# Kernel optimization log

Hardware: AMD Instinct MI355X
Metric: run time of the kernel (lower is better)

Reference implementation:

```python
import jax, jax.numpy as jnp
import numpy as np

DIM = 1024
HEADS = 16
HDIM = DIM // HEADS
HIDDEN = 4 * DIM
SCALE = HDIM ** -0.5


def layernorm(x, g, b, eps=1e-5):
    mu = jnp.mean(x, axis=-1, keepdims=True)
    var = jnp.var(x, axis=-1, keepdims=True)
    return (x - mu) * jax.lax.rsqrt(var + eps) * g + b


def setup_inputs() -> dict:
    key = jax.random.key(0)
    ks = jax.random.split(key, 8)
    s = 0.02
    return {
        "x": jax.random.normal(ks[0], (4, 1024, DIM), dtype=jnp.float32),
        "ln1_g": jnp.ones((DIM,), jnp.float32),
        "ln1_b": jnp.zeros((DIM,), jnp.float32),
        "ln2_g": jnp.ones((DIM,), jnp.float32),
        "ln2_b": jnp.zeros((DIM,), jnp.float32),
        "qkv_w": jax.random.normal(ks[1], (DIM, 3 * DIM), jnp.float32) * s,
        "qkv_b": jnp.zeros((3 * DIM,), jnp.float32),
        "proj_w": jax.random.normal(ks[2], (DIM, DIM), jnp.float32) * s,
        "proj_b": jnp.zeros((DIM,), jnp.float32),
        "fc1_w": jax.random.normal(ks[3], (DIM, HIDDEN), jnp.float32) * s,
        "fc1_b": jnp.zeros((HIDDEN,), jnp.float32),
        "fc2_w": jax.random.normal(ks[4], (HIDDEN, DIM), jnp.float32) * s,
        "fc2_b": jnp.zeros((DIM,), jnp.float32),
    }


def reference(x, ln1_g, ln1_b, ln2_g, ln2_b, qkv_w, qkv_b, proj_w, proj_b,
              fc1_w, fc1_b, fc2_w, fc2_b):
    B, N, C = x.shape
    # --- attention branch ---
    h = layernorm(x, ln1_g, ln1_b)
    qkv = h @ qkv_w + qkv_b                       # [B,N,3C]
    qkv = qkv.reshape(B, N, 3, HEADS, HDIM)
    q, k, v = jnp.moveaxis(qkv, 2, 0)             # each [B,N,H,Dh]
    q = jnp.swapaxes(q, 1, 2)                      # [B,H,N,Dh]
    k = jnp.swapaxes(k, 1, 2)
    v = jnp.swapaxes(v, 1, 2)
    attn = jnp.einsum('bhqd,bhkd->bhqk', q, k) * SCALE
    attn = jax.nn.softmax(attn, axis=-1)
    o = jnp.einsum('bhqk,bhkd->bhqd', attn, v)     # [B,H,N,Dh]
    o = jnp.swapaxes(o, 1, 2).reshape(B, N, C)
    x = x + (o @ proj_w + proj_b)
    # --- MLP branch ---
    h = layernorm(x, ln2_g, ln2_b)
    h = jax.nn.gelu(h @ fc1_w + fc1_b, approximate=False)
    x = x + (h @ fc2_w + fc2_b)
    return x
```

## Files before the change

kernel.cpp:

```cpp
#include <hip/hip_runtime.h>
#include <math.h>

#define DIM    1024
#define HEADS  16
#define HDIM   64
#define HIDDEN 4096
#define BATCH  4
#define SEQ    1024
#define ROWS   (BATCH * SEQ)

typedef short s16x8 __attribute__((ext_vector_type(8)));
typedef float f32x4 __attribute__((ext_vector_type(4)));

__device__ __forceinline__ float blo(unsigned int u) {
    union { unsigned int i; float f; } x; x.i = u << 16; return x.f;
}
__device__ __forceinline__ float bhi(unsigned int u) {
    union { unsigned int i; float f; } x; x.i = u & 0xffff0000u; return x.f;
}
__device__ __forceinline__ unsigned short f2b(float f) {
    union { float f; unsigned int i; } x; x.f = f;
    unsigned int r = x.i + 0x7fffu + ((x.i >> 16) & 1u);
    return (unsigned short)(r >> 16);
}

__device__ __forceinline__ float gelu_f(float x) {
    float z  = fabsf(x) * 0.70710678118f;
    float t  = __builtin_amdgcn_rcpf(__builtin_fmaf(0.3275911f, z, 1.0f));
    float p  = ((((1.061405429f * t - 1.453152027f) * t + 1.421413741f) * t
                 - 0.284496736f) * t + 0.254829592f) * t;
    float e  = exp2f(-0.72134752f * x * x);
    float w  = 0.5f * p * e;
    float phi = (x >= 0.0f) ? (1.0f - w) : w;
    return x * phi;
}

__device__ __forceinline__ size_t tidx(int row, int k, int Kdim) {
    return ((size_t)(row >> 4) * (Kdim >> 5) + (k >> 5)) * 512
         + (size_t)(((k & 31) >> 3) * 128 + (row & 15) * 8 + (k & 7));
}

__device__ __forceinline__ void gload_lds16(const void* g, void* l) {
    __builtin_amdgcn_global_load_lds(
        (const __attribute__((address_space(1))) unsigned int*)g,
        (__attribute__((address_space(3))) unsigned int*)l, 16, 0, 0);
}

__global__ __launch_bounds__(256) void prep_kernel(const float* __restrict__ x,
                                                   const float* __restrict__ g,
                                                   const float* __restrict__ b,
                                                   unsigned short* __restrict__ lnout,
                                                   const float* __restrict__ qkv_w,
                                                   unsigned short* __restrict__ wT_qkv,
                                                   const float* __restrict__ proj_w,
                                                   unsigned short* __restrict__ wT_proj,
                                                   const float* __restrict__ fc1_w,
                                                   unsigned short* __restrict__ wT_fc1,
                                                   const float* __restrict__ fc2_w,
                                                   unsigned short* __restrict__ wT_fc2) {
    __shared__ float red1[256], red2[256];
    __shared__ unsigned short T[64][68];
    const int bid = blockIdx.x;
    const int t = threadIdx.x;

    if (bid < ROWS) {
        int row = bid;
        const float* xr = x + (size_t)row * DIM;
        float4 v = *((const float4*)(xr + t * 4));
        float s  = v.x + v.y + v.z + v.w;
        float ss = v.x * v.x + v.y * v.y + v.z * v.z + v.w * v.w;
        red1[t] = s; red2[t] = ss;
        __syncthreads();
        for (int off = 128; off > 0; off >>= 1) {
            if (t < off) { red1[t] += red1[t + off]; red2[t] += red2[t + off]; }
            __syncthreads();
        }
        float mu   = red1[0] * (1.0f / DIM);
        float var  = red2[0] * (1.0f / DIM) - mu * mu;
        float rstd = rsqrtf(var + 1e-5f);
        float4 gv = *((const float4*)(g + t * 4));
        float4 bv = *((const float4*)(b + t * 4));
        ushort4 o;
        o.x = f2b((v.x - mu) * rstd * gv.x + bv.x);
        o.y = f2b((v.y - mu) * rstd * gv.y + bv.y);
        o.z = f2b((v.z - mu) * rstd * gv.z + bv.z);
        o.w = f2b((v.w - mu) * rstd * gv.w + bv.w);
        *((ushort4*)(lnout + tidx(row, t * 4, DIM))) = o;
    } else {
        int tt = bid - ROWS;
        const float* W; unsigned short* Wt; int K, N, bx, by;
        if (tt < 768) {
            W = qkv_w; Wt = wT_qkv; K = DIM; N = 3 * DIM; bx = tt % 48; by = tt / 48;
        } else if (tt < 768 + 256) {
            tt -= 768;
            W = proj_w; Wt = wT_proj; K = DIM; N = DIM; bx = tt % 16; by = tt / 16;
        } else if (tt < 768 + 256 + 1024) {
            tt -= 768 + 256;
            W = fc1_w; Wt = wT_fc1; K = DIM; N = HIDDEN; bx = tt % 64; by = tt / 64;
        } else {
            tt -= 768 + 256 + 1024;
            W = fc2_w; Wt = wT_fc2; K = HIDDEN; N = DIM; bx = tt % 16; by = tt / 16;
        }
        int n0 = bx * 64, k0 = by * 64;
        int cr = t >> 4;
        int cc = (t & 15) * 4;
        #pragma unroll
        for (int r = 0; r < 4; ++r) {
            int kk = cr + 16 * r;
            float4 v = *((const float4*)(W + (size_t)(k0 + kk) * N + n0 + cc));
            T[cc + 0][kk] = f2b(v.x);
            T[cc + 1][kk] = f2b(v.y);
            T[cc + 2][kk] = f2b(v.z);
            T[cc + 3][kk] = f2b(v.w);
        }
        __syncthreads();
        {
            int nn = t >> 2;
            int kg = (t & 3) * 16;
            #pragma unroll
            for (int p = 0; p < 2; ++p) {
                int k8 = kg + p * 8;
                ushort4 lo = *((ushort4*)&T[nn][k8]);
                ushort4 hi = *((ushort4*)&T[nn][k8 + 4]);
                unsigned short* dst = Wt + tidx(n0 + nn, k0 + k8, K);
                *((ushort4*)dst)       = lo;
                *((ushort4*)(dst + 4)) = hi;
            }
        }
    }
}

__global__ __launch_bounds__(256) void reduce_ln(const unsigned short* __restrict__ p0,
                                                 const unsigned short* __restrict__ p1,
                                                 const float* __restrict__ x,
                                                 const float* __restrict__ bias,
                                                 const float* __restrict__ g,
                                                 const float* __restrict__ b,
                                                 float* __restrict__ xout,
                                                 unsigned short* __restrict__ lnout) {
    int row = blockIdx.x;
    int t = threadIdx.x;
    size_t i = (size_t)row * DIM + t * 4;
    float4 xv = *((const float4*)(x + i));
    float4 bi = *((const float4*)(bias + t * 4));
    uint2 w0 = *((const uint2*)(p0 + i));
    uint2 w1 = *((const uint2*)(p1 + i));
    float4 v;
    v.x = xv.x + bi.x + blo(w0.x) + blo(w1.x);
    v.y = xv.y + bi.y + bhi(w0.x) + bhi(w1.x);
    v.z = xv.z + bi.z + blo(w0.y) + blo(w1.y);
    v.w = xv.w + bi.w + bhi(w0.y) + bhi(w1.y);
    *((float4*)(xout + i)) = v;

    float s  = v.x + v.y + v.z + v.w;
    float ss = v.x * v.x + v.y * v.y + v.z * v.z + v.w * v.w;
    __shared__ float red1[256], red2[256];
    red1[t] = s; red2[t] = ss;
    __syncthreads();
    for (int off = 128; off > 0; off >>= 1) {
        if (t < off) { red1[t] += red1[t + off]; red2[t] += red2[t + off]; }
        __syncthreads();
    }
    float mu   = red1[0] * (1.0f / DIM);
    float var  = red2[0] * (1.0f / DIM) - mu * mu;
    float rstd = rsqrtf(var + 1e-5f);
    float4 gv = *((const float4*)(g + t * 4));
    float4 bv = *((const float4*)(b + t * 4));
    ushort4 o;
    o.x = f2b((v.x - mu) * rstd * gv.x + bv.x);
    o.y = f2b((v.y - mu) * rstd * gv.y + bv.y);
    o.z = f2b((v.z - mu) * rstd * gv.z + bv.z);
    o.w = f2b((v.w - mu) * rstd * gv.w + bv.w);
    *((ushort4*)(lnout + tidx(row, t * 4, DIM))) = o;
}

__global__ __launch_bounds__(256, 4) void mfma_gemm(const unsigned short* __restrict__ A,
                                                 const unsigned short* __restrict__ Bt,
                                                 const float* __restrict__ bias,
                                                 void* __restrict__ Cout,
                                                 unsigned short* __restrict__ vt,
                                                 unsigned short* __restrict__ p0,
                                                 unsigned short* __restrict__ p1,
                                                 unsigned short* __restrict__ p2,
                                                 unsigned short* __restrict__ p3,
                                                 int M, int N, int K, int Ksplit, int fuse) {
    __shared__ __align__(16) short Asm[2][4096];
    __shared__ __align__(16) short Bsm[2][4096];

    const int tid  = threadIdx.x;
    const int lane = tid & 63;
    const int wave = tid >> 6;
    const int wy = wave >> 1, wx = wave & 1;
    const int lr = lane & 15;
    const int lq = lane >> 4;

    int m_t, n_t;
    {
        const int mt = gridDim.x, ntl = gridDim.y, G = 8;
        if (ntl > G) {
            int lin = blockIdx.y * mt + blockIdx.x;
            int gsz = mt * G;
            int grp = lin / gsz;
            int rem = lin - grp * gsz;
            m_t = rem % mt;
            n_t = grp * G + rem / mt;
        } else { m_t = blockIdx.x; n_t = blockIdx.y; }
    }
    const int m0 = m_t * 128, n0 = n_t * 128;
    const int kbase = blockIdx.z * Ksplit;
    const int kch = K >> 5;

    f32x4 acc[4][4];
    #pragma unroll
    for (int i = 0; i < 4; ++i)
        #pragma unroll
        for (int j = 0; j < 4; ++j)
            acc[i][j] = (f32x4){0.f, 0.f, 0.f, 0.f};

    const unsigned short* ag[2]; const unsigned short* bg[2];
    #pragma unroll
    for (int j = 0; j < 2; ++j) {
        int rc = wave * 2 + j;
        ag[j] = A  + ((size_t)((m0 >> 4) + rc) * kch + (kbase >> 5)) * 512 + lane * 8;
        bg[j] = Bt + ((size_t)((n0 >> 4) + rc) * kch + (kbase >> 5)) * 512 + lane * 8;
    }

#define STAGE(buf) { \
    _Pragma("unroll") for (int j_ = 0; j_ < 2; ++j_) { \
        gload_lds16(ag[j_], &Asm[buf][(wave * 2 + j_) * 512]); \
        gload_lds16(bg[j_], &Bsm[buf][(wave * 2 + j_) * 512]); \
        ag[j_] += 512; bg[j_] += 512; \
    } }
#define COMPUTE(buf) { \
    s16x8 af[4], bf[4]; \
    _Pragma("unroll") for (int i_ = 0; i_ < 4; ++i_) \
        af[i_] = *((const s16x8*)&Asm[buf][(wy * 4 + i_) * 512 + lane * 8]); \
    _Pragma("unroll") for (int j_ = 0; j_ < 4; ++j_) \
        bf[j_] = *((const s16x8*)&Bsm[buf][(wx * 4 + j_) * 512 + lane * 8]); \
    _Pragma("unroll") for (int i_ = 0; i_ < 4; ++i_) \
        _Pragma("unroll") for (int j_ = 0; j_ < 4; ++j_) \
            acc[i_][j_] = __builtin_amdgcn_mfma_f32_16x16x32_bf16(af[i_], bf[j_], acc[i_][j_], 0, 0, 0); \
    }

    STAGE(0);
    __syncthreads();
    for (int k0 = 0; k0 < Ksplit; k0 += 64) {
        STAGE(1);
        COMPUTE(0);
        __syncthreads();
        if (k0 + 64 < Ksplit) STAGE(0);
        COMPUTE(1);
        __syncthreads();
    }
#undef STAGE
#undef COMPUTE

    short* Wl = (wave < 2 ? (short*)Asm : (short*)Bsm) + (wave & 1) * 4096;

    if (fuse == 0 && vt && (n0 + wx * 64) >= 2 * DIM) {
        #pragma unroll
        for (int j = 0; j < 4; ++j) {
            int col = n0 + wx * 64 + j * 16 + lr;
            float bi = bias[col];
            #pragma unroll
            for (int i = 0; i < 4; ++i) {
                int row0 = m0 + wy * 64 + i * 16 + lq * 4;
                #pragma unroll
                for (int r = 0; r < 4; ++r) {
                    float val = acc[i][j][r] + bi;
                    int row = row0 + r;
                    int b_ = row >> 10, tok = row & 1023;
                    int hd = col - 2 * DIM, h_ = hd >> 6, d = hd & 63;
                    size_t o = (size_t)(b_ * 16 + h_) * 65536
                             + ((size_t)(d >> 4) * 32 + (tok >> 5)) * 512
                             + ((tok & 31) >> 3) * 128 + (d & 15) * 8 + (tok & 7);
                    vt[o] = f2b(val);
                }
            }
        }
    } else if (fuse == 3) {
        #pragma unroll
        for (int j = 0; j < 4; ++j) {
            #pragma unroll
            for (int i = 0; i < 4; ++i) {
                #pragma unroll
                for (int r = 0; r < 4; ++r) {
                    int rowL = i * 16 + lq * 4 + r;
                    int colL = (j * 16 + lr) ^ ((rowL & 7) << 3);
                    Wl[rowL * 64 + colL] = (short)f2b(acc[i][j][r]);
                }
            }
        }
        int z = blockIdx.z;
        unsigned short* P = (z == 0) ? p0 : (z == 1) ? p1 : (z == 2) ? p2 : p3;
        unsigned short* Prow = P + (size_t)(m0 + wy * 64 + lane) * N + n0 + wx * 64;
        #pragma unroll
        for (int c = 0; c < 8; ++c) {
            int colr = (c * 8) ^ ((lane & 7) << 3);
            s16x8 v = *((const s16x8*)&Wl[lane * 64 + colr]);
            *((s16x8*)&Prow[c * 8]) = v;
        }
    } else {
        #pragma unroll
        for (int j = 0; j < 4; ++j) {
            float bi = bias[n0 + wx * 64 + j * 16 + lr];
            #pragma unroll
            for (int i = 0; i < 4; ++i) {
                #pragma unroll
                for (int r = 0; r < 4; ++r) {
                    float val = acc[i][j][r] + bi;
                    if (fuse == 1) val = gelu_f(val);
                    int colL = (j & 1) * 16 + lr;
                    int hi = colL >> 3;
                    int pos = hi * 128 + (lq * 4 + r) * 8 + (lr & 7);
                    pos ^= ((pos >> 7) & 3) << 3;
                    Wl[(i * 2 + (j >> 1)) * 512 + pos] = (short)f2b(val);
                }
            }
        }
        const size_t rc0 = (size_t)((m0 + wy * 64) >> 4);
        const size_t cc0 = (size_t)((n0 + wx * 64) >> 5);
        const size_t nch = (size_t)(N >> 5);
        #pragma unroll
        for (int c = 0; c < 8; ++c) {
            int raddr = lane * 8;
            raddr ^= ((raddr >> 7) & 3) << 3;
            s16x8 v = *((const s16x8*)&Wl[c * 512 + raddr]);
            size_t chunk = (rc0 + (c >> 1)) * nch + cc0 + (c & 1);
            *((s16x8*)&((unsigned short*)Cout)[chunk * 512 + lane * 8]) = v;
        }
    }
}

__global__ __launch_bounds__(256) void reduce_kernel(const unsigned short* __restrict__ p0,
                                                     const unsigned short* __restrict__ p1,
                                                     const unsigned short* __restrict__ p2,
                                                     const unsigned short* __restrict__ p3,
                                                     int S,
                                                     const float* __restrict__ x,
                                                     const float* __restrict__ bias,
                                                     float* __restrict__ out) {
    int i = (blockIdx.x * 256 + threadIdx.x) * 8;
    int col = i & (DIM - 1);
    float4 b0 = *((const float4*)(bias + col));
    float4 b1 = *((const float4*)(bias + col + 4));
    float4 x0 = *((const float4*)(x + i));
    float4 x1 = *((const float4*)(x + i + 4));
    float a[8] = {x0.x + b0.x, x0.y + b0.y, x0.z + b0.z, x0.w + b0.w,
                  x1.x + b1.x, x1.y + b1.y, x1.z + b1.z, x1.w + b1.w};
    const unsigned short* ps[4] = {p0, p1, p2, p3};
    for (int s = 0; s < S; ++s) {
        uint4 w = *((const uint4*)(ps[s] + i));
        a[0] += blo(w.x); a[1] += bhi(w.x);
        a[2] += blo(w.y); a[3] += bhi(w.y);
        a[4] += blo(w.z); a[5] += bhi(w.z);
        a[6] += blo(w.w); a[7] += bhi(w.w);
    }
    *((float4*)(out + i))     = make_float4(a[0], a[1], a[2], a[3]);
    *((float4*)(out + i + 4)) = make_float4(a[4], a[5], a[6], a[7]);
}

__global__ __launch_bounds__(256, 6) void fattn_mfma(const unsigned short* __restrict__ qkv,
                                                  const unsigned short* __restrict__ Vt,
                                                  unsigned short* __restrict__ out) {
    __shared__ __align__(16) short Ks[4096];
    __shared__ __align__(16) short Vs[4096];
    __shared__ __align__(16) short Ps[64 * 72];
    __shared__ __align__(16) short OnesB[512];

    const int tid = threadIdx.x, lane = tid & 63, wave = tid >> 6;
    const int lr = lane & 15, lq = lane >> 4;
    const int L = blockIdx.x;
    const int idx = L >> 3;
    const int qt = idx & 15;
    const int bh = (L & 7) + 8 * (idx >> 4);
    const int b = bh >> 4, h = bh & 15;
    const int q0 = qt * 64;

    {
        s16x8 z = (s16x8){0,0,0,0,0,0,0,0};
        if (lr == 0) { z[0] = (short)0x3F80; z[1] = (short)0x3F80;
                       z[2] = (short)0x3F80; z[3] = (short)0x3F80;
                       z[4] = (short)0x3F80; z[5] = (short)0x3F80;
                       z[6] = (short)0x3F80; z[7] = (short)0x3F80; }
        if (wave == 0) *((s16x8*)&OnesB[lane * 8]) = z;
    }

    s16x8 aq[2];
    #pragma unroll
    for (int j = 0; j < 2; ++j) {
        const unsigned short* g = qkv + ((size_t)(((b * SEQ + q0) >> 4) + wave) * 96
                                         + 2 * h + j) * 512 + lane * 8;
        aq[j] = *((const s16x8*)g);
    }

    const unsigned short* kg_[2]; const unsigned short* vg_[2];
    short *kl_[2], *vl_[2];
    #pragma unroll
    for (int j = 0; j < 2; ++j) {
        int cid = wave * 2 + j;
        kg_[j] = qkv + ((size_t)(((b * SEQ) >> 4) + (cid >> 1)) * 96
                        + 32 + 2 * h + (cid & 1)) * 512 + lane * 8;
        vg_[j] = Vt + (size_t)bh * 65536
                 + ((size_t)(cid >> 1) * 32 + (cid & 1)) * 512 + lane * 8;
        kl_[j] = &Ks[cid * 512];
        vl_[j] = &Vs[cid * 512];
    }

    f32x4 osum[5];
    #pragma unroll
    for (int d = 0; d < 5; ++d)
        osum[d] = (f32x4){0.f, 0.f, 0.f, 0.f};

    const float c = 0.125f * 1.44269504f;

    for (int k0 = 0; k0 < SEQ; k0 += 64) {
        #pragma unroll
        for (int j = 0; j < 2; ++j) {
            gload_lds16(kg_[j], kl_[j]);
            gload_lds16(vg_[j], vl_[j]);
            kg_[j] += 4 * 96 * 512;
            vg_[j] += 1024;
        }
        __syncthreads();

        f32x4 s[4];
        #pragma unroll
        for (int jb = 0; jb < 4; ++jb)
            s[jb] = (f32x4){0.f, 0.f, 0.f, 0.f};
        __builtin_amdgcn_s_setprio(1);
        #pragma unroll
        for (int kc = 0; kc < 2; ++kc) {
            #pragma unroll
            for (int jb = 0; jb < 4; ++jb) {
                s16x8 bk = *((const s16x8*)&Ks[(jb * 2 + kc) * 512 + lane * 8]);
                s[jb] = __builtin_amdgcn_mfma_f32_16x16x32_bf16(aq[kc], bk, s[jb], 0, 0, 0);
            }
        }
        __builtin_amdgcn_s_setprio(0);

        #pragma unroll
        for (int r = 0; r < 4; ++r) {
            int prow = wave * 16 + lq * 4 + r;
            #pragma unroll
            for (int jb = 0; jb < 4; ++jb)
                Ps[prow * 72 + jb * 16 + lr] = (short)f2b(exp2f(s[jb][r] * c));
        }

        __builtin_amdgcn_s_setprio(1);
        #pragma unroll
        for (int kc = 0; kc < 2; ++kc) {
            s16x8 ap = *((const s16x8*)&Ps[(wave * 16 + lr) * 72 + kc * 32 + lq * 8]);
            #pragma unroll
            for (int db = 0; db < 4; ++db) {
                s16x8 bv = *((const s16x8*)&Vs[(db * 2 + kc) * 512 + lane * 8]);
                osum[db] = __builtin_amdgcn_mfma_f32_16x16x32_bf16(ap, bv, osum[db], 0, 0, 0);
            }
            s16x8 bo = *((const s16x8*)&OnesB[lane * 8]);
            osum[4] = __builtin_amdgcn_mfma_f32_16x16x32_bf16(ap, bo, osum[4], 0, 0, 0);
        }
        __builtin_amdgcn_s_setprio(0);
        __syncthreads();
    }

    {
        int qrow = q0 + wave * 16 + lq * 4;
        #pragma unroll
        for (int r = 0; r < 4; ++r) {
            float lsum = __shfl(osum[4][r], lane & 48, 64);
            float inv = 1.0f / lsum;
            int row = b * SEQ + qrow + r;
            #pragma unroll
            for (int db = 0; db < 4; ++db)
                out[tidx(row, h * 64 + db * 16 + lr, DIM)] = f2b(osum[db][r] * inv);
        }
    }
}

extern "C" void kernel_launch(void* const* d_in, const int* in_sizes, int n_in,
                              void* d_out, int out_size, void* d_ws, size_t ws_size,
                              hipStream_t stream) {
    const float* x      = (const float*)d_in[0];
    const float* ln1_g  = (const float*)d_in[1];
    const float* ln1_b  = (const float*)d_in[2];
    const float* ln2_g  = (const float*)d_in[3];
    const float* ln2_b  = (const float*)d_in[4];
    const float* qkv_w  = (const float*)d_in[5];
    const float* qkv_b  = (const float*)d_in[6];
    const float* proj_w = (const float*)d_in[7];
    const float* proj_b = (const float*)d_in[8];
    const float* fc1_w  = (const float*)d_in[9];
    const float* fc1_b  = (const float*)d_in[10];
    const float* fc2_w  = (const float*)d_in[11];
    const float* fc2_b  = (const float*)d_in[12];
    float* out = (float*)d_out;

    char* ws = (char*)d_ws;
    unsigned short* wT_fc2  = (unsigned short*)(ws);
    unsigned short* wT_qkv  = (unsigned short*)(ws + (8u  << 20));
    unsigned short* wT_proj = (unsigned short*)(ws + (14u << 20));
    unsigned short* qkvbuf  = (unsigned short*)(ws + (16u << 20));
    unsigned short* Vt      = (unsigned short*)(ws + (40u << 20));
    unsigned short* attnout = (unsigned short*)(ws + (48u << 20));
    unsigned short* lnout   = (unsigned short*)(ws + (56u << 20));
    unsigned short* wT_fc1  = (unsigned short*)(ws + (64u << 20));
    unsigned short* gelu    = (unsigned short*)(ws + (16u << 20));
    unsigned short* pp0 = (unsigned short*)(ws + (16u << 20));
    unsigned short* pp1 = (unsigned short*)(ws + (24u << 20));
    unsigned short* fp0 = (unsigned short*)(ws + (48u << 20));
    unsigned short* fp1 = (unsigned short*)(ws + (56u << 20));
    unsigned short* fp2 = (unsigned short*)(ws + (64u << 20));
    unsigned short* fp3 = (unsigned short*)(ws + (8u  << 20));

    prep_kernel<<<ROWS + 3072, 256, 0, stream>>>(
        x, ln1_g, ln1_b, lnout,
        qkv_w, wT_qkv, proj_w, wT_proj, fc1_w, wT_fc1, fc2_w, wT_fc2);
    mfma_gemm<<<dim3(ROWS / 128, 3 * DIM / 128, 1), 256, 0, stream>>>(
        lnout, wT_qkv, qkv_b, qkvbuf, Vt, nullptr, nullptr, nullptr, nullptr,
        ROWS, 3 * DIM, DIM, DIM, 0);
    fattn_mfma<<<(SEQ / 64) * BATCH * HEADS, 256, 0, stream>>>(qkvbuf, Vt, attnout);
    mfma_gemm<<<dim3(ROWS / 128, DIM / 128, 2), 256, 0, stream>>>(
        attnout, wT_proj, proj_b, nullptr, nullptr, pp0, pp1, nullptr, nullptr,
        ROWS, DIM, DIM, DIM / 2, 3);
    reduce_ln<<<ROWS, 256, 0, stream>>>(pp0, pp1, x, proj_b, ln2_g, ln2_b, out, lnout);
    mfma_gemm<<<dim3(ROWS / 128, HIDDEN / 128, 1), 256, 0, stream>>>(
        lnout, wT_fc1, fc1_b, gelu, nullptr, nullptr, nullptr, nullptr, nullptr,
        ROWS, HIDDEN, DIM, DIM, 1);
    mfma_gemm<<<dim3(ROWS / 128, DIM / 128, 4), 256, 0, stream>>>(
        gelu, wT_fc2, fc2_b, nullptr, nullptr, fp0, fp1, fp2, fp3,
        ROWS, DIM, HIDDEN, HIDDEN / 4, 3);
    reduce_kernel<<<ROWS * DIM / 2048, 256, 0, stream>>>(
        fp0, fp1, fp2, fp3, 4, out, fc2_b, out);
}
```

Measured before the change: 332.8 us.

## Atomic split-K fc2 epilogue, LDS-staged V store, double-buffered 32-key attention

```diff
diff --git a/kernel.cpp b/kernel.cpp
--- a/kernel.cpp
+++ b/kernel.cpp
@@ -181,8 +181,6 @@
                                                  unsigned short* __restrict__ vt,
                                                  unsigned short* __restrict__ p0,
                                                  unsigned short* __restrict__ p1,
-                                                 unsigned short* __restrict__ p2,
-                                                 unsigned short* __restrict__ p3,
                                                  int M, int N, int K, int Ksplit, int fuse) {
     __shared__ __align__(16) short Asm[2][4096];
     __shared__ __align__(16) short Bsm[2][4096];
@@ -258,24 +256,43 @@
     short* Wl = (wave < 2 ? (short*)Asm : (short*)Bsm) + (wave & 1) * 4096;
 
     if (fuse == 0 && vt && (n0 + wx * 64) >= 2 * DIM) {
+        int b_ = (m0 + wy * 64) >> 10;
+        int tok0 = (m0 + wy * 64) & 1023;
+        int h_ = (n0 + wx * 64 - 2 * DIM) >> 6;
+        #pragma unroll
+        for (int j = 0; j < 4; ++j) {
+            float bi = bias[n0 + wx * 64 + j * 16 + lr];
+            #pragma unroll
+            for (int i = 0; i < 4; ++i) {
+                #pragma unroll
+                for (int r = 0; r < 4; ++r) {
+                    float val = acc[i][j][r] + bi;
+                    int tl = i * 16 + lq * 4 + r;
+                    int c  = j * 2 + (i >> 1);
+                    int pos = ((tl & 31) >> 3) * 128 + lr * 8 + (tl & 7);
+                    Wl[c * 512 + pos] = (short)f2b(val);
+                }
+            }
+        }
+        unsigned short* vbase = vt + (size_t)(b_ * 16 + h_) * 65536;
+        #pragma unroll
+        for (int c = 0; c < 8; ++c) {
+            s16x8 v = *((const s16x8*)&Wl[c * 512 + lane * 8]);
+            size_t off = ((size_t)(c >> 1) * 32 + (tok0 >> 5) + (c & 1)) * 512 + lane * 8;
+            *((s16x8*)&vbase[off]) = v;
+        }
+    } else if (fuse == 2) {
+        float* O = (float*)Cout;
         #pragma unroll
         for (int j = 0; j < 4; ++j) {
             int col = n0 + wx * 64 + j * 16 + lr;
-            float bi = bias[col];
+            float bi = (blockIdx.z == 0) ? bias[col] : 0.f;
             #pragma unroll
             for (int i = 0; i < 4; ++i) {
                 int row0 = m0 + wy * 64 + i * 16 + lq * 4;
                 #pragma unroll
-                for (int r = 0; r < 4; ++r) {
-                    float val = acc[i][j][r] + bi;
-                    int row = row0 + r;
-                    int b_ = row >> 10, tok = row & 1023;
-                    int hd = col - 2 * DIM, h_ = hd >> 6, d = hd & 63;
-                    size_t o = (size_t)(b_ * 16 + h_) * 65536
-                             + ((size_t)(d >> 4) * 32 + (tok >> 5)) * 512
-                             + ((tok & 31) >> 3) * 128 + (d & 15) * 8 + (tok & 7);
-                    vt[o] = f2b(val);
-                }
+                for (int r = 0; r < 4; ++r)
+                    atomicAdd(&O[(size_t)(row0 + r) * N + col], acc[i][j][r] + bi);
             }
         }
     } else if (fuse == 3) {
@@ -291,8 +308,7 @@
                 }
             }
         }
-        int z = blockIdx.z;
-        unsigned short* P = (z == 0) ? p0 : (z == 1) ? p1 : (z == 2) ? p2 : p3;
+        unsigned short* P = (blockIdx.z == 0) ? p0 : p1;
         unsigned short* Prow = P + (size_t)(m0 + wy * 64 + lane) * N + n0 + wx * 64;
         #pragma unroll
         for (int c = 0; c < 8; ++c) {
@@ -332,40 +348,12 @@
     }
 }
 
-__global__ __launch_bounds__(256) void reduce_kernel(const unsigned short* __restrict__ p0,
-                                                     const unsigned short* __restrict__ p1,
-                                                     const unsigned short* __restrict__ p2,
-                                                     const unsigned short* __restrict__ p3,
-                                                     int S,
-                                                     const float* __restrict__ x,
-                                                     const float* __restrict__ bias,
-                                                     float* __restrict__ out) {
-    int i = (blockIdx.x * 256 + threadIdx.x) * 8;
-    int col = i & (DIM - 1);
-    float4 b0 = *((const float4*)(bias + col));
-    float4 b1 = *((const float4*)(bias + col + 4));
-    float4 x0 = *((const float4*)(x + i));
-    float4 x1 = *((const float4*)(x + i + 4));
-    float a[8] = {x0.x + b0.x, x0.y + b0.y, x0.z + b0.z, x0.w + b0.w,
-                  x1.x + b1.x, x1.y + b1.y, x1.z + b1.z, x1.w + b1.w};
-    const unsigned short* ps[4] = {p0, p1, p2, p3};
-    for (int s = 0; s < S; ++s) {
-        uint4 w = *((const uint4*)(ps[s] + i));
-        a[0] += blo(w.x); a[1] += bhi(w.x);
-        a[2] += blo(w.y); a[3] += bhi(w.y);
-        a[4] += blo(w.z); a[5] += bhi(w.z);
-        a[6] += blo(w.w); a[7] += bhi(w.w);
-    }
-    *((float4*)(out + i))     = make_float4(a[0], a[1], a[2], a[3]);
-    *((float4*)(out + i + 4)) = make_float4(a[4], a[5], a[6], a[7]);
-}
-
 __global__ __launch_bounds__(256, 6) void fattn_mfma(const unsigned short* __restrict__ qkv,
                                                   const unsigned short* __restrict__ Vt,
                                                   unsigned short* __restrict__ out) {
-    __shared__ __align__(16) short Ks[4096];
-    __shared__ __align__(16) short Vs[4096];
-    __shared__ __align__(16) short Ps[64 * 72];
+    __shared__ __align__(16) short Ks[2][2048];
+    __shared__ __align__(16) short Vs[2][2048];
+    __shared__ __align__(16) short Ps[64 * 40];
     __shared__ __align__(16) short OnesB[512];
 
     const int tid = threadIdx.x, lane = tid & 63, wave = tid >> 6;
@@ -394,18 +382,9 @@
         aq[j] = *((const s16x8*)g);
     }
 
-    const unsigned short* kg_[2]; const unsigned short* vg_[2];
-    short *kl_[2], *vl_[2];
-    #pragma unroll
-    for (int j = 0; j < 2; ++j) {
-        int cid = wave * 2 + j;
-        kg_[j] = qkv + ((size_t)(((b * SEQ) >> 4) + (cid >> 1)) * 96
-                        + 32 + 2 * h + (cid & 1)) * 512 + lane * 8;
-        vg_[j] = Vt + (size_t)bh * 65536
-                 + ((size_t)(cid >> 1) * 32 + (cid & 1)) * 512 + lane * 8;
-        kl_[j] = &Ks[cid * 512];
-        vl_[j] = &Vs[cid * 512];
-    }
+    const unsigned short* kgb = qkv + ((size_t)(((b * SEQ) >> 4) + (wave >> 1)) * 96
+                                       + 32 + 2 * h + (wave & 1)) * 512 + lane * 8;
+    const unsigned short* vgb = Vt + (size_t)bh * 65536 + (size_t)wave * 32 * 512 + lane * 8;
 
     f32x4 osum[5];
     #pragma unroll
@@ -414,54 +393,48 @@
 
     const float c = 0.125f * 1.44269504f;
 
-    for (int k0 = 0; k0 < SEQ; k0 += 64) {
-        #pragma unroll
-        for (int j = 0; j < 2; ++j) {
-            gload_lds16(kg_[j], kl_[j]);
-            gload_lds16(vg_[j], vl_[j]);
-            kg_[j] += 4 * 96 * 512;
-            vg_[j] += 1024;
-        }
-        __syncthreads();
-
-        f32x4 s[4];
-        #pragma unroll
-        for (int jb = 0; jb < 4; ++jb)
-            s[jb] = (f32x4){0.f, 0.f, 0.f, 0.f};
-        __builtin_amdgcn_s_setprio(1);
-        #pragma unroll
-        for (int kc = 0; kc < 2; ++kc) {
-            #pragma unroll
-            for (int jb = 0; jb < 4; ++jb) {
-                s16x8 bk = *((const s16x8*)&Ks[(jb * 2 + kc) * 512 + lane * 8]);
-                s[jb] = __builtin_amdgcn_mfma_f32_16x16x32_bf16(aq[kc], bk, s[jb], 0, 0, 0);
-            }
-        }
-        __builtin_amdgcn_s_setprio(0);
-
-        #pragma unroll
-        for (int r = 0; r < 4; ++r) {
-            int prow = wave * 16 + lq * 4 + r;
-            #pragma unroll
-            for (int jb = 0; jb < 4; ++jb)
-                Ps[prow * 72 + jb * 16 + lr] = (short)f2b(exp2f(s[jb][r] * c));
-        }
-
-        __builtin_amdgcn_s_setprio(1);
-        #pragma unroll
-        for (int kc = 0; kc < 2; ++kc) {
-            s16x8 ap = *((const s16x8*)&Ps[(wave * 16 + lr) * 72 + kc * 32 + lq * 8]);
-            #pragma unroll
-            for (int db = 0; db < 4; ++db) {
-                s16x8 bv = *((const s16x8*)&Vs[(db * 2 + kc) * 512 + lane * 8]);
-                osum[db] = __builtin_amdgcn_mfma_f32_16x16x32_bf16(ap, bv, osum[db], 0, 0, 0);
-            }
-            s16x8 bo = *((const s16x8*)&OnesB[lane * 8]);
-            osum[4] = __builtin_amdgcn_mfma_f32_16x16x32_bf16(ap, bo, osum[4], 0, 0, 0);
-        }
-        __builtin_amdgcn_s_setprio(0);
-        __syncthreads();
-    }
+#define ASTG(buf, kt) { \
+    gload_lds16(kgb + (size_t)(kt) * (2 * 96 * 512), &Ks[buf][wave * 512]); \
+    gload_lds16(vgb + (size_t)(kt) * 512, &Vs[buf][wave * 512]); }
+
+#define ACMP(buf) { \
+    f32x4 s0 = (f32x4){0.f,0.f,0.f,0.f}, s1 = (f32x4){0.f,0.f,0.f,0.f}; \
+    __builtin_amdgcn_s_setprio(1); \
+    _Pragma("unroll") for (int kc_ = 0; kc_ < 2; ++kc_) { \
+        s16x8 bk0 = *((const s16x8*)&Ks[buf][(0 * 2 + kc_) * 512 + lane * 8]); \
+        s16x8 bk1 = *((const s16x8*)&Ks[buf][(1 * 2 + kc_) * 512 + lane * 8]); \
+        s0 = __builtin_amdgcn_mfma_f32_16x16x32_bf16(aq[kc_], bk0, s0, 0, 0, 0); \
+        s1 = __builtin_amdgcn_mfma_f32_16x16x32_bf16(aq[kc_], bk1, s1, 0, 0, 0); \
+    } \
+    __builtin_amdgcn_s_setprio(0); \
+    _Pragma("unroll") for (int r_ = 0; r_ < 4; ++r_) { \
+        int prow = wave * 16 + lq * 4 + r_; \
+        Ps[prow * 40 + lr]      = (short)f2b(exp2f(s0[r_] * c)); \
+        Ps[prow * 40 + 16 + lr] = (short)f2b(exp2f(s1[r_] * c)); \
+    } \
+    s16x8 ap = *((const s16x8*)&Ps[(wave * 16 + lr) * 40 + lq * 8]); \
+    __builtin_amdgcn_s_setprio(1); \
+    _Pragma("unroll") for (int db_ = 0; db_ < 4; ++db_) { \
+        s16x8 bv = *((const s16x8*)&Vs[buf][db_ * 512 + lane * 8]); \
+        osum[db_] = __builtin_amdgcn_mfma_f32_16x16x32_bf16(ap, bv, osum[db_], 0, 0, 0); \
+    } \
+    osum[4] = __builtin_amdgcn_mfma_f32_16x16x32_bf16(ap, bo, osum[4], 0, 0, 0); \
+    __builtin_amdgcn_s_setprio(0); }
+
+    ASTG(0, 0);
+    __syncthreads();
+    s16x8 bo = *((const s16x8*)&OnesB[lane * 8]);
+
+    for (int t = 0; t < 32; t += 2) {
+        ASTG(1, t + 1);
+        ACMP(0);
+        __syncthreads();
+        if (t + 2 < 32) ASTG(0, t + 2);
+        ACMP(1);
+        __syncthreads();
+    }
+#undef ASTG
+#undef ACMP
 
     {
         int qrow = q0 + wave * 16 + lq * 4;
@@ -507,28 +480,22 @@
     unsigned short* gelu    = (unsigned short*)(ws + (16u << 20));
     unsigned short* pp0 = (unsigned short*)(ws + (16u << 20));
     unsigned short* pp1 = (unsigned short*)(ws + (24u << 20));
-    unsigned short* fp0 = (unsigned short*)(ws + (48u << 20));
-    unsigned short* fp1 = (unsigned short*)(ws + (56u << 20));
-    unsigned short* fp2 = (unsigned short*)(ws + (64u << 20));
-    unsigned short* fp3 = (unsigned short*)(ws + (8u  << 20));
 
     prep_kernel<<<ROWS + 3072, 256, 0, stream>>>(
         x, ln1_g, ln1_b, lnout,
         qkv_w, wT_qkv, proj_w, wT_proj, fc1_w, wT_fc1, fc2_w, wT_fc2);
     mfma_gemm<<<dim3(ROWS / 128, 3 * DIM / 128, 1), 256, 0, stream>>>(
-        lnout, wT_qkv, qkv_b, qkvbuf, Vt, nullptr, nullptr, nullptr, nullptr,
+        lnout, wT_qkv, qkv_b, qkvbuf, Vt, nullptr, nullptr,
         ROWS, 3 * DIM, DIM, DIM, 0);
     fattn_mfma<<<(SEQ / 64) * BATCH * HEADS, 256, 0, stream>>>(qkvbuf, Vt, attnout);
     mfma_gemm<<<dim3(ROWS / 128, DIM / 128, 2), 256, 0, stream>>>(
-        attnout, wT_proj, proj_b, nullptr, nullptr, pp0, pp1, nullptr, nullptr,
+        attnout, wT_proj, proj_b, nullptr, nullptr, pp0, pp1,
         ROWS, DIM, DIM, DIM / 2, 3);
     reduce_ln<<<ROWS, 256, 0, stream>>>(pp0, pp1, x, proj_b, ln2_g, ln2_b, out, lnout);
     mfma_gemm<<<dim3(ROWS / 128, HIDDEN / 128, 1), 256, 0, stream>>>(
-        lnout, wT_fc1, fc1_b, gelu, nullptr, nullptr, nullptr, nullptr, nullptr,
+        lnout, wT_fc1, fc1_b, gelu, nullptr, nullptr, nullptr,
         ROWS, HIDDEN, DIM, DIM, 1);
     mfma_gemm<<<dim3(ROWS / 128, DIM / 128, 4), 256, 0, stream>>>(
-        gelu, wT_fc2, fc2_b, nullptr, nullptr, fp0, fp1, fp2, fp3,
-        ROWS, DIM, HIDDEN, HIDDEN / 4, 3);
-    reduce_kernel<<<ROWS * DIM / 2048, 256, 0, stream>>>(
-        fp0, fp1, fp2, fp3, 4, out, fc2_b, out);
-}
+        gelu, wT_fc2, fc2_b, out, nullptr, nullptr, nullptr,
+        ROWS, DIM, HIDDEN, HIDDEN / 4, 2);
+}
```

Result: slower. 353.8 us (+6.3%).
